# Performance work log

Hardware: AMD Instinct MI355X
Metric: run time of the kernel (lower is better)

## Reference

```python
import jax, jax.numpy as jnp
import numpy as np

ALPHA = 0.2  # LeakyReLU negative slope


def _gat_layer(x, xq, src, dst, W_l, a_l, N):
    # x, xq: [N, Din]; W_l: [Din, D]; a_l: [2*D]
    h = x @ W_l            # [N, D]
    hq = xq @ W_l          # [N, D]
    D = W_l.shape[1]
    # a @ cat(hq[src], h[dst]) splits into two per-node dot products
    sq = hq @ a_l[:D]      # [N]
    sn = h @ a_l[D:]       # [N]
    s = sq[src] + sn[dst]  # [E]
    e = jnp.exp(-jnp.where(s >= 0, s, ALPHA * s))          # [E]
    rowsum = jax.ops.segment_sum(e, src, num_segments=N)    # [N]
    agg = jax.ops.segment_sum(e[:, None] * h[dst], src, num_segments=N)  # [N, D]
    denom = jnp.where(rowsum == 0, 1.0, rowsum)[:, None]
    h_prime = agg / denom
    # torch replaces NaN (0/0) with 0; isolated nodes -> 0
    return jnp.where(rowsum[:, None] == 0, 0.0, h_prime)


def setup_inputs() -> dict:
    key = jax.random.key(0)
    k1, k2, k3, k4, k5 = jax.random.split(key, 5)
    B, N, D, E, L = 2, 20000, 256, 320000, 2
    nodes = jax.random.normal(k1, (B, N, D), dtype=jnp.float32)
    nodes_query = jax.random.normal(k2, (B, N, D), dtype=jnp.float32)
    W = jax.random.normal(k3, (L, D, D), dtype=jnp.float32) * 0.088  # xavier_normal gain=1.414
    a = jax.random.normal(k4, (L, 2 * D), dtype=jnp.float32) * 0.074
    edges = jax.random.randint(k5, (B, 2, E), 0, N, dtype=jnp.int32)
    return {"nodes": nodes, "nodes_query": nodes_query, "W": W, "a": a, "edges": edges}


def reference(nodes, nodes_query, W, a, edges):
    B, N, D = nodes.shape
    L = W.shape[0]

    def per_graph(x, xq, e):
        src, dst = e[0], e[1]
        h = x
        for l in range(L):  # small fixed layer count
            h = _gat_layer(h, xq, src, dst, W[l], a[l], N)
        return h

    out = jax.vmap(per_graph)(nodes, nodes_query, edges)
    return out + nodes  # residual
```

## Files before the change

kernel.cpp:

```cpp
#include <hip/hip_runtime.h>
#include <hip/hip_fp16.h>
#include <math.h>

constexpr int N = 20000, D = 256, E = 320000, B = 2, L = 2;
constexpr int CAP = 64;

typedef __bf16 bf16x8 __attribute__((ext_vector_type(8)));
typedef float f32x4 __attribute__((ext_vector_type(4)));

__device__ __forceinline__ unsigned short f2bf(float f) {
  unsigned int u = __float_as_uint(f);
  u = (u + 0x7FFF + ((u >> 16) & 1)) >> 16;
  return (unsigned short)u;
}
__device__ __forceinline__ unsigned short f2h(float f) {
  __half h = __float2half(f);
  return *(unsigned short*)&h;
}
__device__ __forceinline__ float2 h2f(unsigned int u) {
  __half2 hv = *reinterpret_cast<__half2*>(&u);
  return __half22float2(hv);
}

__global__ __launch_bounds__(256) void prep_kernel(const float* __restrict__ W,
                                                   const float* __restrict__ a,
                                                   unsigned short* __restrict__ Wt,
                                                   float* __restrict__ wa,
                                                   uint4* __restrict__ zbase) {
  int bi = blockIdx.x, tid = threadIdx.x;
  if (bi < 512) {
    __shared__ float t[16][17];
    int l = bi >> 8, rem = bi & 255;
    int by = rem >> 4, bx = rem & 15;
    int tx = tid & 15, ty = tid >> 4;
    t[ty][tx] = W[l * 65536 + (by * 16 + ty) * 256 + bx * 16 + tx];
    __syncthreads();
    Wt[l * 65536 + (bx * 16 + ty) * 256 + by * 16 + tx] = f2bf(t[tx][ty]);
  } else if (bi < 514) {
    int l = bi - 512;
    float s = 0.f;
    for (int d = 0; d < D; ++d) s += W[l * 65536 + tid * D + d] * a[l * 2 * D + d];
    wa[l * D + tid] = s;
  } else {
    int zi = (bi - 514) * 256 + tid;
    if (zi < 30000) zbase[zi] = make_uint4(0, 0, 0, 0);
  }
}

__global__ __launch_bounds__(256) void tsc_kernel(const float* __restrict__ nodes,
                                                  unsigned short* __restrict__ nbf,
                                                  const float* __restrict__ xq,
                                                  const float* __restrict__ wa,
                                                  float* __restrict__ sq,
                                                  const int* __restrict__ edges,
                                                  int* __restrict__ deg,
                                                  int* __restrict__ slot) {
  int bi = blockIdx.x, tid = threadIdx.x;
  if (bi < 2500) {
    int e = bi * 256 + tid;
    int b = (e >= E) ? 1 : 0;
    int s = edges[(size_t)b * E + e];
    int d = edges[(size_t)(b + 1) * E + e];
    int nb = b * N + s;
    int pos = atomicAdd(&deg[nb], 1);
    if (pos < CAP) slot[((size_t)nb << 6) + pos] = d;
  } else if (bi < 7500) {
    int i = (bi - 2500) * 256 + tid;
    float4 v0 = ((const float4*)nodes)[i * 2];
    float4 v1 = ((const float4*)nodes)[i * 2 + 1];
    unsigned short t[8] = {f2bf(v0.x), f2bf(v0.y), f2bf(v0.z), f2bf(v0.w),
                           f2bf(v1.x), f2bf(v1.y), f2bf(v1.z), f2bf(v1.w)};
    ((uint4*)nbf)[i] = *(uint4*)t;
  } else {
    int sqb = bi - 7500;
    int b = (sqb >= 5000) ? 1 : 0;
    int blk = sqb - b * 5000;
    int wave = blk * 4 + (tid >> 6);
    int lane = tid & 63;
    const float4 xv = *(const float4*)(xq + ((size_t)b * N + wave) * D + (lane << 2));
    const float4 w0 = *(const float4*)(wa + (lane << 2));
    const float4 w1 = *(const float4*)(wa + D + (lane << 2));
    float s0 = xv.x * w0.x + xv.y * w0.y + xv.z * w0.z + xv.w * w0.w;
    float s1 = xv.x * w1.x + xv.y * w1.y + xv.z * w1.z + xv.w * w1.w;
    for (int off = 32; off; off >>= 1) {
      s0 += __shfl_down(s0, off);
      s1 += __shfl_down(s1, off);
    }
    if (lane == 0) {
      sq[(b * 2 + 0) * N + wave] = s0;
      sq[(b * 2 + 1) * N + wave] = s1;
    }
  }
}

__global__ __launch_bounds__(256) void gemm_mfma(const unsigned short* __restrict__ A,
                                                 const unsigned short* __restrict__ Wt,
                                                 unsigned short* __restrict__ Ch,
                                                 const float* __restrict__ a2,
                                                 float* __restrict__ sn, int M) {
  __shared__ unsigned short As[128 * 32];
  __shared__ unsigned short Bs[64 * 32];
  int z = blockIdx.z;
  const unsigned short* Az = A + (size_t)z * M * 256;
  unsigned short* Cz = Ch + (size_t)z * M * 256;
  float* snz = sn + (size_t)z * M;
  int tid = threadIdx.x;
  int bm = blockIdx.y * 128, bn = blockIdx.x * 64;
  int wv = tid >> 6, lane = tid & 63;
  int lm = lane & 15, lq = lane >> 4;
  f32x4 acc[2][4] = {};

  for (int k0 = 0; k0 < 256; k0 += 32) {
    int m = tid >> 1, kb = (tid & 1) << 4;
    if (bm + m < M) {
      const unsigned short* ap = Az + (size_t)(bm + m) * 256 + k0 + kb;
      *(uint4*)&As[m * 32 + kb] = *(const uint4*)ap;
      *(uint4*)&As[m * 32 + kb + 8] = *(const uint4*)(ap + 8);
    } else {
      uint4 z4 = make_uint4(0, 0, 0, 0);
      *(uint4*)&As[m * 32 + kb] = z4;
      *(uint4*)&As[m * 32 + kb + 8] = z4;
    }
    int nn = tid >> 2, kb2 = (tid & 3) << 3;
    *(uint4*)&Bs[nn * 32 + kb2] = *(const uint4*)(Wt + (size_t)(bn + nn) * 256 + k0 + kb2);
    __syncthreads();

    bf16x8 af0 = *(const bf16x8*)&As[(wv * 32 + lm) * 32 + lq * 8];
    bf16x8 af1 = *(const bf16x8*)&As[(wv * 32 + 16 + lm) * 32 + lq * 8];
#pragma unroll
    for (int nf = 0; nf < 4; ++nf) {
      bf16x8 bfr = *(const bf16x8*)&Bs[(nf * 16 + lm) * 32 + lq * 8];
      acc[0][nf] = __builtin_amdgcn_mfma_f32_16x16x32_bf16(af0, bfr, acc[0][nf], 0, 0, 0);
      acc[1][nf] = __builtin_amdgcn_mfma_f32_16x16x32_bf16(af1, bfr, acc[1][nf], 0, 0, 0);
    }
    __syncthreads();
  }

  float a2v[4];
#pragma unroll
  for (int nf = 0; nf < 4; ++nf) a2v[nf] = a2[bn + nf * 16 + lm];
#pragma unroll
  for (int f = 0; f < 2; ++f) {
#pragma unroll
    for (int r = 0; r < 4; ++r) {
      int row = bm + wv * 32 + f * 16 + lq * 4 + r;
      if (row < M) {
        float partial = 0.f;
#pragma unroll
        for (int nf = 0; nf < 4; ++nf) {
          float v = acc[f][nf][r];
          Cz[(size_t)row * 256 + bn + nf * 16 + lm] = f2h(v);
          partial += v * a2v[nf];
        }
        partial += __shfl_xor(partial, 1);
        partial += __shfl_xor(partial, 2);
        partial += __shfl_xor(partial, 4);
        partial += __shfl_xor(partial, 8);
        if (lm == 0) atomicAdd(&snz[row], partial);
      }
    }
  }
}

__global__ __launch_bounds__(256) void agg_kernel(const int* __restrict__ deg,
                                                  const int* __restrict__ slot,
                                                  const float* __restrict__ sq_all,
                                                  const float* __restrict__ sn,
                                                  const unsigned short* __restrict__ hhf,
                                                  const float* __restrict__ resid,
                                                  float* __restrict__ outf,
                                                  unsigned short* __restrict__ outbf, int l) {
  int b = blockIdx.y;
  int tid = threadIdx.x, wv = tid >> 6, lane = tid & 63;
  int node = blockIdx.x * 4 + wv;
  int eg = lane >> 5, dl = lane & 31;
  const float* snb = sn + (size_t)b * N;
  const unsigned short* hb = hhf + (size_t)b * N * 256;
  int nb = b * N + node;
  int cnt = min(deg[nb], CAP);
  const int* sl = slot + ((size_t)nb << 6);
  float sqv = sq_all[((b << 1) + l) * N + node];
  int idx = 0;
  float snv = 0.f;
  if (lane < cnt) {
    idx = sl[lane];
    snv = snb[idx];
  }
  int nj = (cnt - eg + 1) >> 1;
  uint4 hv[4];
#pragma unroll
  for (int u = 0; u < 4; ++u) {
    int dsti = __shfl(idx, eg + 2 * u);
    if (u < nj) hv[u] = *(const uint4*)(hb + (size_t)dsti * 256 + (dl << 3));
  }
  float s = sqv + snv;
  float lr = (s >= 0.f) ? s : 0.2f * s;
  float w = (lane < cnt) ? __expf(-lr) : 0.f;
  float wsum = w;
  float acc[8] = {};
  for (int u0 = 0; u0 < nj; u0 += 4) {
    uint4 hn[4];
#pragma unroll
    for (int u = 0; u < 4; ++u) {
      int uu = u0 + 4 + u;
      int js = eg + 2 * uu;
      js = (js < 63) ? js : 63;
      int dsti = __shfl(idx, js);
      if (uu < nj) hn[u] = *(const uint4*)(hb + (size_t)dsti * 256 + (dl << 3));
    }
#pragma unroll
    for (int u = 0; u < 4; ++u) {
      int uu = u0 + u;
      if (uu < nj) {
        float wj = __shfl(w, eg + 2 * uu);
        float2 f0 = h2f(hv[u].x), f1 = h2f(hv[u].y), f2 = h2f(hv[u].z), f3 = h2f(hv[u].w);
        acc[0] = fmaf(wj, f0.x, acc[0]);
        acc[1] = fmaf(wj, f0.y, acc[1]);
        acc[2] = fmaf(wj, f1.x, acc[2]);
        acc[3] = fmaf(wj, f1.y, acc[3]);
        acc[4] = fmaf(wj, f2.x, acc[4]);
        acc[5] = fmaf(wj, f2.y, acc[5]);
        acc[6] = fmaf(wj, f3.x, acc[6]);
        acc[7] = fmaf(wj, f3.y, acc[7]);
      }
    }
#pragma unroll
    for (int u = 0; u < 4; ++u) hv[u] = hn[u];
  }
  for (int off = 32; off; off >>= 1) wsum += __shfl_xor(wsum, off);
#pragma unroll
  for (int i = 0; i < 8; ++i) acc[i] += __shfl_xor(acc[i], 32);
  float inv = (wsum > 0.f) ? 1.f / wsum : 0.f;
  float o0 = (eg ? acc[4] : acc[0]) * inv;
  float o1 = (eg ? acc[5] : acc[1]) * inv;
  float o2 = (eg ? acc[6] : acc[2]) * inv;
  float o3 = (eg ? acc[7] : acc[3]) * inv;
  size_t rowoff = ((size_t)b * N + node) * 256 + (dl << 3) + (eg << 2);
  if (outbf) {
    unsigned short t[4] = {f2bf(o0), f2bf(o1), f2bf(o2), f2bf(o3)};
    *(uint2*)(outbf + rowoff) = *(uint2*)t;
  } else {
    const float4 rv = *(const float4*)(resid + rowoff);
    *(float4*)(outf + rowoff) = make_float4(o0 + rv.x, o1 + rv.y, o2 + rv.z, o3 + rv.w);
  }
}

extern "C" void kernel_launch(void* const* d_in, const int* in_sizes, int n_in,
                              void* d_out, int out_size, void* d_ws, size_t ws_size,
                              hipStream_t stream) {
  const float* nodes = (const float*)d_in[0];
  const float* nodesq = (const float*)d_in[1];
  const float* W = (const float*)d_in[2];
  const float* a = (const float*)d_in[3];
  const int* edges = (const int*)d_in[4];
  float* out = (float*)d_out;

  const size_t ND = (size_t)N * D;
  unsigned short* hhf = (unsigned short*)d_ws;
  unsigned short* h1bf = hhf + (size_t)B * ND;
  unsigned short* nbf = h1bf + (size_t)B * ND;
  unsigned short* Wt = nbf + (size_t)B * ND;
  float* sn0 = (float*)(Wt + (size_t)L * D * D);
  float* sn1 = sn0 + B * N;
  int* deg = (int*)(sn1 + B * N);
  float* sq_all = (float*)(deg + B * N);
  float* wa = sq_all + (size_t)B * L * N;
  int* slot = (int*)(wa + L * D);

  prep_kernel<<<632, 256, 0, stream>>>(W, a, Wt, wa, (uint4*)sn0);
  tsc_kernel<<<17500, 256, 0, stream>>>(nodes, nbf, nodesq, wa, sq_all, edges, deg, slot);

  for (int l = 0; l < L; ++l) {
    const float* al2 = a + (size_t)l * 2 * D + D;
    const unsigned short* Acur = (l == 0) ? nbf : h1bf;
    float* snl = (l == 0) ? sn0 : sn1;
    gemm_mfma<<<dim3(4, (N + 127) / 128, B), 256, 0, stream>>>(Acur, Wt + (size_t)l * D * D,
                                                               hhf, al2, snl, N);
    bool last = (l == L - 1);
    agg_kernel<<<dim3(N / 4, B), 256, 0, stream>>>(deg, slot, sq_all, snl, hhf,
                                                   last ? nodes : nullptr,
                                                   last ? out : nullptr,
                                                   last ? nullptr : h1bf, l);
  }
}
```

Measured before the change: 289.0 us.

## Fuse fp32-to-fp16 input conversion into first GEMM and switch MFMA to fp16

Removes the separate pass that converted the node features to bf16 and instead loads fp32 rows inside the layer-0 GEMM, converting them to fp16 in registers before the shared-memory store. All GEMM operands, weights and intermediate activations move from bf16 to fp16 MFMA. The edge-bucketing section now handles four edges per thread, which cuts its block count. This saves one full read/write of the node tensor and a workspace buffer, at the cost of doubled global A-tile traffic in the layer-0 GEMM and fp16 range limits.

```diff
diff --git a/kernel.cpp b/kernel.cpp
--- a/kernel.cpp
+++ b/kernel.cpp
@@ -5,14 +5,9 @@
 constexpr int N = 20000, D = 256, E = 320000, B = 2, L = 2;
 constexpr int CAP = 64;
 
-typedef __bf16 bf16x8 __attribute__((ext_vector_type(8)));
+typedef _Float16 f16x8 __attribute__((ext_vector_type(8)));
 typedef float f32x4 __attribute__((ext_vector_type(4)));
 
-__device__ __forceinline__ unsigned short f2bf(float f) {
-  unsigned int u = __float_as_uint(f);
-  u = (u + 0x7FFF + ((u >> 16) & 1)) >> 16;
-  return (unsigned short)u;
-}
 __device__ __forceinline__ unsigned short f2h(float f) {
   __half h = __float2half(f);
   return *(unsigned short*)&h;
@@ -35,7 +30,7 @@
     int tx = tid & 15, ty = tid >> 4;
     t[ty][tx] = W[l * 65536 + (by * 16 + ty) * 256 + bx * 16 + tx];
     __syncthreads();
-    Wt[l * 65536 + (bx * 16 + ty) * 256 + by * 16 + tx] = f2bf(t[tx][ty]);
+    Wt[l * 65536 + (bx * 16 + ty) * 256 + by * 16 + tx] = f2h(t[tx][ty]);
   } else if (bi < 514) {
     int l = bi - 512;
     float s = 0.f;
@@ -47,32 +42,33 @@
   }
 }
 
-__global__ __launch_bounds__(256) void tsc_kernel(const float* __restrict__ nodes,
-                                                  unsigned short* __restrict__ nbf,
-                                                  const float* __restrict__ xq,
+__global__ __launch_bounds__(256) void tsc_kernel(const float* __restrict__ xq,
                                                   const float* __restrict__ wa,
                                                   float* __restrict__ sq,
                                                   const int* __restrict__ edges,
                                                   int* __restrict__ deg,
                                                   int* __restrict__ slot) {
   int bi = blockIdx.x, tid = threadIdx.x;
-  if (bi < 2500) {
-    int e = bi * 256 + tid;
-    int b = (e >= E) ? 1 : 0;
-    int s = edges[(size_t)b * E + e];
-    int d = edges[(size_t)(b + 1) * E + e];
-    int nb = b * N + s;
-    int pos = atomicAdd(&deg[nb], 1);
-    if (pos < CAP) slot[((size_t)nb << 6) + pos] = d;
-  } else if (bi < 7500) {
-    int i = (bi - 2500) * 256 + tid;
-    float4 v0 = ((const float4*)nodes)[i * 2];
-    float4 v1 = ((const float4*)nodes)[i * 2 + 1];
-    unsigned short t[8] = {f2bf(v0.x), f2bf(v0.y), f2bf(v0.z), f2bf(v0.w),
-                           f2bf(v1.x), f2bf(v1.y), f2bf(v1.z), f2bf(v1.w)};
-    ((uint4*)nbf)[i] = *(uint4*)t;
+  if (bi < 625) {
+    int ebase = bi * 1024 + tid;
+    int s4[4], d4[4];
+#pragma unroll
+    for (int q = 0; q < 4; ++q) {
+      int e = ebase + q * 256;
+      int b = (e >= E) ? 1 : 0;
+      s4[q] = edges[(size_t)b * E + e];
+      d4[q] = edges[(size_t)(b + 1) * E + e];
+    }
+#pragma unroll
+    for (int q = 0; q < 4; ++q) {
+      int e = ebase + q * 256;
+      int b = (e >= E) ? 1 : 0;
+      int nb = b * N + s4[q];
+      int pos = atomicAdd(&deg[nb], 1);
+      if (pos < CAP) slot[((size_t)nb << 6) + pos] = d4[q];
+    }
   } else {
-    int sqb = bi - 7500;
+    int sqb = bi - 625;
     int b = (sqb >= 5000) ? 1 : 0;
     int blk = sqb - b * 5000;
     int wave = blk * 4 + (tid >> 6);
@@ -93,7 +89,8 @@
   }
 }
 
-__global__ __launch_bounds__(256) void gemm_mfma(const unsigned short* __restrict__ A,
+template <bool F32A>
+__global__ __launch_bounds__(256) void gemm_mfma(const void* __restrict__ Av,
                                                  const unsigned short* __restrict__ Wt,
                                                  unsigned short* __restrict__ Ch,
                                                  const float* __restrict__ a2,
@@ -101,7 +98,6 @@
   __shared__ unsigned short As[128 * 32];
   __shared__ unsigned short Bs[64 * 32];
   int z = blockIdx.z;
-  const unsigned short* Az = A + (size_t)z * M * 256;
   unsigned short* Cz = Ch + (size_t)z * M * 256;
   float* snz = sn + (size_t)z * M;
   int tid = threadIdx.x;
@@ -113,9 +109,24 @@
   for (int k0 = 0; k0 < 256; k0 += 32) {
     int m = tid >> 1, kb = (tid & 1) << 4;
     if (bm + m < M) {
-      const unsigned short* ap = Az + (size_t)(bm + m) * 256 + k0 + kb;
-      *(uint4*)&As[m * 32 + kb] = *(const uint4*)ap;
-      *(uint4*)&As[m * 32 + kb + 8] = *(const uint4*)(ap + 8);
+      if constexpr (F32A) {
+        const float* ap = (const float*)Av + (size_t)z * M * 256 + (size_t)(bm + m) * 256 + k0 + kb;
+        float4 v0 = ((const float4*)ap)[0];
+        float4 v1 = ((const float4*)ap)[1];
+        float4 v2 = ((const float4*)ap)[2];
+        float4 v3 = ((const float4*)ap)[3];
+        unsigned short t[16] = {f2h(v0.x), f2h(v0.y), f2h(v0.z), f2h(v0.w),
+                                f2h(v1.x), f2h(v1.y), f2h(v1.z), f2h(v1.w),
+                                f2h(v2.x), f2h(v2.y), f2h(v2.z), f2h(v2.w),
+                                f2h(v3.x), f2h(v3.y), f2h(v3.z), f2h(v3.w)};
+        *(uint4*)&As[m * 32 + kb] = *(uint4*)t;
+        *(uint4*)&As[m * 32 + kb + 8] = *(uint4*)(t + 8);
+      } else {
+        const unsigned short* ap =
+            (const unsigned short*)Av + (size_t)z * M * 256 + (size_t)(bm + m) * 256 + k0 + kb;
+        *(uint4*)&As[m * 32 + kb] = *(const uint4*)ap;
+        *(uint4*)&As[m * 32 + kb + 8] = *(const uint4*)(ap + 8);
+      }
     } else {
       uint4 z4 = make_uint4(0, 0, 0, 0);
       *(uint4*)&As[m * 32 + kb] = z4;
@@ -125,13 +136,13 @@
     *(uint4*)&Bs[nn * 32 + kb2] = *(const uint4*)(Wt + (size_t)(bn + nn) * 256 + k0 + kb2);
     __syncthreads();
 
-    bf16x8 af0 = *(const bf16x8*)&As[(wv * 32 + lm) * 32 + lq * 8];
-    bf16x8 af1 = *(const bf16x8*)&As[(wv * 32 + 16 + lm) * 32 + lq * 8];
+    f16x8 af0 = *(const f16x8*)&As[(wv * 32 + lm) * 32 + lq * 8];
+    f16x8 af1 = *(const f16x8*)&As[(wv * 32 + 16 + lm) * 32 + lq * 8];
 #pragma unroll
     for (int nf = 0; nf < 4; ++nf) {
-      bf16x8 bfr = *(const bf16x8*)&Bs[(nf * 16 + lm) * 32 + lq * 8];
-      acc[0][nf] = __builtin_amdgcn_mfma_f32_16x16x32_bf16(af0, bfr, acc[0][nf], 0, 0, 0);
-      acc[1][nf] = __builtin_amdgcn_mfma_f32_16x16x32_bf16(af1, bfr, acc[1][nf], 0, 0, 0);
+      f16x8 bfr = *(const f16x8*)&Bs[(nf * 16 + lm) * 32 + lq * 8];
+      acc[0][nf] = __builtin_amdgcn_mfma_f32_16x16x32_f16(af0, bfr, acc[0][nf], 0, 0, 0);
+      acc[1][nf] = __builtin_amdgcn_mfma_f32_16x16x32_f16(af1, bfr, acc[1][nf], 0, 0, 0);
     }
     __syncthreads();
   }
@@ -169,7 +180,7 @@
                                                   const unsigned short* __restrict__ hhf,
                                                   const float* __restrict__ resid,
                                                   float* __restrict__ outf,
-                                                  unsigned short* __restrict__ outbf, int l) {
+                                                  unsigned short* __restrict__ outh, int l) {
   int b = blockIdx.y;
   int tid = threadIdx.x, wv = tid >> 6, lane = tid & 63;
   int node = blockIdx.x * 4 + wv;
@@ -236,9 +247,9 @@
   float o2 = (eg ? acc[6] : acc[2]) * inv;
   float o3 = (eg ? acc[7] : acc[3]) * inv;
   size_t rowoff = ((size_t)b * N + node) * 256 + (dl << 3) + (eg << 2);
-  if (outbf) {
-    unsigned short t[4] = {f2bf(o0), f2bf(o1), f2bf(o2), f2bf(o3)};
-    *(uint2*)(outbf + rowoff) = *(uint2*)t;
+  if (outh) {
+    unsigned short t[4] = {f2h(o0), f2h(o1), f2h(o2), f2h(o3)};
+    *(uint2*)(outh + rowoff) = *(uint2*)t;
   } else {
     const float4 rv = *(const float4*)(resid + rowoff);
     *(float4*)(outf + rowoff) = make_float4(o0 + rv.x, o1 + rv.y, o2 + rv.z, o3 + rv.w);
@@ -257,9 +268,8 @@
 
   const size_t ND = (size_t)N * D;
   unsigned short* hhf = (unsigned short*)d_ws;
-  unsigned short* h1bf = hhf + (size_t)B * ND;
-  unsigned short* nbf = h1bf + (size_t)B * ND;
-  unsigned short* Wt = nbf + (size_t)B * ND;
+  unsigned short* h1hf = hhf + (size_t)B * ND;
+  unsigned short* Wt = h1hf + (size_t)B * ND;
   float* sn0 = (float*)(Wt + (size_t)L * D * D);
   float* sn1 = sn0 + B * N;
   int* deg = (int*)(sn1 + B * N);
@@ -268,18 +278,22 @@
   int* slot = (int*)(wa + L * D);
 
   prep_kernel<<<632, 256, 0, stream>>>(W, a, Wt, wa, (uint4*)sn0);
-  tsc_kernel<<<17500, 256, 0, stream>>>(nodes, nbf, nodesq, wa, sq_all, edges, deg, slot);
+  tsc_kernel<<<10625, 256, 0, stream>>>(nodesq, wa, sq_all, edges, deg, slot);
 
   for (int l = 0; l < L; ++l) {
     const float* al2 = a + (size_t)l * 2 * D + D;
-    const unsigned short* Acur = (l == 0) ? nbf : h1bf;
     float* snl = (l == 0) ? sn0 : sn1;
-    gemm_mfma<<<dim3(4, (N + 127) / 128, B), 256, 0, stream>>>(Acur, Wt + (size_t)l * D * D,
-                                                               hhf, al2, snl, N);
     bool last = (l == L - 1);
+    if (l == 0) {
+      gemm_mfma<true><<<dim3(4, (N + 127) / 128, B), 256, 0, stream>>>(
+          nodes, Wt, hhf, al2, snl, N);
+    } else {
+      gemm_mfma<false><<<dim3(4, (N + 127) / 128, B), 256, 0, stream>>>(
+          h1hf, Wt + (size_t)D * D, hhf, al2, snl, N);
+    }
     agg_kernel<<<dim3(N / 4, B), 256, 0, stream>>>(deg, slot, sq_all, snl, hhf,
                                                    last ? nodes : nullptr,
                                                    last ? out : nullptr,
-                                                   last ? nullptr : h1bf, l);
-  }
-}
+                                                   last ? nullptr : h1hf, l);
+  }
+}
```

New measurement: 299.1 us. 1.03x slower.
